# Kernel tuning notes

Measured on AMD Instinct MI355X. Metric: run time of the kernel, lower is better.

## Reference

```python
import jax, jax.numpy as jnp
import numpy as np

NEG_SLOPE = 0.2  # PyG GATConv default negative_slope
NUM_GRAPHS = 64


def gat_conv(x, src, dst, W, a_src, a_dst, bias, concat):
    """PyG-style GATConv (eval mode, self-loops already appended to src/dst)."""
    N = x.shape[0]
    H, C = a_src.shape
    h = (x @ W).reshape(N, H, C)                      # [N,H,C]
    al_s = jnp.sum(h * a_src, axis=-1)                # [N,H]
    al_d = jnp.sum(h * a_dst, axis=-1)                # [N,H]
    e = jax.nn.leaky_relu(al_s[src] + al_d[dst], NEG_SLOPE)  # [E,H]
    # numerically-stable segment softmax over incoming edges of each dst node
    m = jax.ops.segment_max(e, dst, num_segments=N)   # [N,H]
    ex = jnp.exp(e - m[dst])
    denom = jax.ops.segment_sum(ex, dst, num_segments=N)
    alpha = ex / (denom[dst] + 1e-16)                 # [E,H]
    out = jax.ops.segment_sum(h[src] * alpha[:, :, None], dst, num_segments=N)  # [N,H,C]
    out = out.reshape(N, H * C) if concat else out.mean(axis=1)
    return out + bias


def setup_inputs() -> dict:
    key = jax.random.key(0)
    ks = jax.random.split(key, 32)
    N, E, F_in, H = 20000, 100000, 128, 8
    x = jax.random.normal(ks[0], (N, F_in), jnp.float32)
    edge_index = jax.random.randint(ks[1], (2, E), 0, N, dtype=jnp.int32)
    batch = jnp.sort(jax.random.randint(ks[2], (N,), 0, NUM_GRAPHS, dtype=jnp.int32))
    inp = {"x": x, "edge_index": edge_index, "batch": batch}
    # (fan_in, per-head channels) for conv1..conv_final
    dims = [(F_in, 64), (512, 256), (2048, 256), (2048, 256), (2048, 256)]
    ki = 3
    for i, (fi, c) in enumerate(dims, 1):
        concat = i < 5
        inp[f"W{i}"] = jax.random.normal(ks[ki], (fi, H * c), jnp.float32) * (1.0 / np.sqrt(fi)); ki += 1
        inp[f"a_src{i}"] = jax.random.normal(ks[ki], (H, c), jnp.float32) * 0.1; ki += 1
        inp[f"a_dst{i}"] = jax.random.normal(ks[ki], (H, c), jnp.float32) * 0.1; ki += 1
        inp[f"b{i}"] = jnp.zeros((H * c if concat else c,), jnp.float32)
    inp["W_lin"] = jax.random.normal(ks[ki], (256, 128), jnp.float32) * (1.0 / np.sqrt(256))
    inp["b_lin"] = jnp.zeros((128,), jnp.float32)
    return inp


def reference(x, edge_index, batch,
              W1, a_src1, a_dst1, b1,
              W2, a_src2, a_dst2, b2,
              W3, a_src3, a_dst3, b3,
              W4, a_src4, a_dst4, b4,
              W5, a_src5, a_dst5, b5,
              W_lin, b_lin):
    N = x.shape[0]
    loop = jnp.arange(N, dtype=edge_index.dtype)  # GATConv add_self_loops=True
    src = jnp.concatenate([edge_index[0], loop])
    dst = jnp.concatenate([edge_index[1], loop])
    h = jax.nn.elu(gat_conv(x, src, dst, W1, a_src1, a_dst1, b1, True))
    h = jax.nn.elu(gat_conv(h, src, dst, W2, a_src2, a_dst2, b2, True))
    h = jax.nn.elu(gat_conv(h, src, dst, W3, a_src3, a_dst3, b3, True))
    h = jax.nn.elu(gat_conv(h, src, dst, W4, a_src4, a_dst4, b4, True))
    h = jax.nn.elu(gat_conv(h, src, dst, W5, a_src5, a_dst5, b5, False))
    sums = jax.ops.segment_sum(h, batch, num_segments=NUM_GRAPHS)
    counts = jax.ops.segment_sum(jnp.ones((N, 1), h.dtype), batch, num_segments=NUM_GRAPHS)
    pooled = jax.nn.elu(sums / jnp.maximum(counts, 1.0))  # global_mean_pool + elu
    return pooled @ W_lin + b_lin
```

## Files before the change

### kernel.cpp

```cpp
#include <hip/hip_runtime.h>
#include <hip/hip_fp16.h>
#include <math.h>

#define NHEADS 8
#define NG 64

typedef _Float16 half8_t __attribute__((ext_vector_type(8)));
typedef _Float16 half4_t __attribute__((ext_vector_type(4)));
typedef float    float4_t __attribute__((ext_vector_type(4)));
typedef __attribute__((address_space(1))) const void g_void;
typedef __attribute__((address_space(3))) void l_void;

__device__ __forceinline__ float elu_f(float x)   { return x > 0.f ? x : expf(x) - 1.f; }
__device__ __forceinline__ float lrelu_f(float x) { return x >= 0.f ? x : 0.2f * x; }

__device__ __forceinline__ float4 ld4(const float* p) { return *(const float4*)p; }
__device__ __forceinline__ float4 ld4(const __half* p) {
    const __half2* q = (const __half2*)p;
    __half2 a = q[0], b = q[1];
    return make_float4(__half2float(a.x), __half2float(a.y),
                       __half2float(b.x), __half2float(b.y));
}
__device__ __forceinline__ void st4(float* p, float4 v) { *(float4*)p = v; }
__device__ __forceinline__ void st4(__half* p, float4 v) {
    __half2 a, b;
    a.x = __float2half(v.x); a.y = __float2half(v.y);
    b.x = __float2half(v.z); b.y = __float2half(v.w);
    __half2* q = (__half2*)p; q[0] = a; q[1] = b;
}
__device__ __forceinline__ float scl(float v)  { return v; }
__device__ __forceinline__ float scl(__half v) { return __half2float(v); }
__device__ __forceinline__ void sst(float* p, float v)  { *p = v; }
__device__ __forceinline__ void sst(__half* p, float v) { *p = __float2half(v); }

__global__ void hist_kernel(const int* __restrict__ ei, int E, int Etot, int* __restrict__ counts) {
    int e = blockIdx.x * blockDim.x + threadIdx.x;
    if (e >= Etot) return;
    int dst = (e < E) ? ei[E + e] : (e - E);
    atomicAdd(&counts[dst], 1);
}

__global__ void scan_kernel(const int* __restrict__ counts, int* __restrict__ offsets,
                            int* __restrict__ cursor, int N) {
    __shared__ int sdata[256];
    __shared__ int carry_s;
    if (threadIdx.x == 0) carry_s = 0;
    __syncthreads();
    for (int base = 0; base < N; base += 256) {
        int i = base + (int)threadIdx.x;
        int v = (i < N) ? counts[i] : 0;
        sdata[threadIdx.x] = v;
        __syncthreads();
        for (int off = 1; off < 256; off <<= 1) {
            int t = (threadIdx.x >= (unsigned)off) ? sdata[threadIdx.x - off] : 0;
            __syncthreads();
            sdata[threadIdx.x] += t;
            __syncthreads();
        }
        int excl = sdata[threadIdx.x] - v + carry_s;
        if (i < N) { offsets[i] = excl; cursor[i] = excl; }
        __syncthreads();
        if (threadIdx.x == 255) carry_s += sdata[255];
        __syncthreads();
    }
    if (threadIdx.x == 0) offsets[N] = carry_s;
}

__global__ void scatter_kernel(const int* __restrict__ ei, int E, int Etot,
                               int* __restrict__ cursor, int* __restrict__ perm_src) {
    int e = blockIdx.x * blockDim.x + threadIdx.x;
    if (e >= Etot) return;
    int src, dst;
    if (e < E) { src = ei[e]; dst = ei[E + e]; }
    else       { src = e - E; dst = e - E; }
    int pos = atomicAdd(&cursor[dst], 1);
    perm_src[pos] = src;
}

__global__ __launch_bounds__(256) void transpose_conv_kernel(const float* __restrict__ W,
                                                             __half* __restrict__ Wt,
                                                             int K, int N) {
    __shared__ float t[32][33];
    int nb = blockIdx.x * 32, kb = blockIdx.y * 32;
    int tx = threadIdx.x & 31, ty = threadIdx.x >> 5;
#pragma unroll
    for (int r = 0; r < 32; r += 8)
        t[ty + r][tx] = W[(size_t)(kb + ty + r) * N + nb + tx];
    __syncthreads();
#pragma unroll
    for (int r = 0; r < 32; r += 8)
        Wt[(size_t)(nb + ty + r) * K + kb + tx] = __float2half(t[tx][ty + r]);
}

struct h4s { __half a, b, c, d; };
__global__ void f32_to_f16_kernel(const float* __restrict__ in, __half* __restrict__ out, long n4) {
    long i = (long)blockIdx.x * blockDim.x + threadIdx.x;
    if (i >= n4) return;
    float4 v = ((const float4*)in)[i];
    h4s o; o.a = __float2half(v.x); o.b = __float2half(v.y);
    o.c = __float2half(v.z); o.d = __float2half(v.w);
    ((h4s*)out)[i] = o;
}

__global__ __launch_bounds__(256) void gemm_mfma_kernel(const __half* __restrict__ A,
                                                        const __half* __restrict__ Bt,
                                                        __half* __restrict__ C,
                                                        int M, int N, int K) {
    __shared__ __align__(16) __half Asm[128 * 64];
    __shared__ __align__(16) __half Bsm[128 * 64];
    const int tid  = threadIdx.x;
    const int lane = tid & 63;
    const int wave = tid >> 6;

    const int nwg = (int)(gridDim.x * gridDim.y);
    const int lin = (int)(blockIdx.y * gridDim.x + blockIdx.x);
    const int q = nwg >> 3, r = nwg & 7;
    const int xcd = lin & 7, idx = lin >> 3;
    const int nid = (xcd < r ? xcd * (q + 1) : r * (q + 1) + (xcd - r) * q) + idx;
    const int bx = nid % (int)gridDim.x;
    const int by = nid / (int)gridDim.x;
    const int row0 = by * 128;
    const int col0 = bx * 128;

    const int l15 = lane & 15;
    const int l4  = lane >> 4;
    const int wm  = (wave >> 1) * 64;
    const int wn  = (wave & 1) * 64;

    const int sl_row = lane >> 3;
    const int sl_kch = (lane & 7) ^ sl_row;

    float4_t acc[4][4];
#pragma unroll
    for (int i = 0; i < 4; ++i)
#pragma unroll
        for (int j = 0; j < 4; ++j)
            acc[i][j] = (float4_t){0.f, 0.f, 0.f, 0.f};

    for (int k0 = 0; k0 < K; k0 += 64) {
#pragma unroll
        for (int i = 0; i < 4; ++i) {
            int rr = (i * 4 + wave) * 8 + sl_row;
            int ar = row0 + rr; if (ar >= M) ar = M - 1;
            const __half* ga = A + (size_t)ar * K + k0 + sl_kch * 8;
            char* la = (char*)Asm + ((i * 4 + wave) * 1024 + lane * 16);
            __builtin_amdgcn_global_load_lds((g_void*)ga, (l_void*)la, 16, 0, 0);
            const __half* gb = Bt + (size_t)(col0 + rr) * K + k0 + sl_kch * 8;
            char* lb = (char*)Bsm + ((i * 4 + wave) * 1024 + lane * 16);
            __builtin_amdgcn_global_load_lds((g_void*)gb, (l_void*)lb, 16, 0, 0);
        }
        __syncthreads();
#pragma unroll
        for (int kh = 0; kh < 2; ++kh) {
            half8_t af[4], bf[4];
#pragma unroll
            for (int f = 0; f < 4; ++f) {
                int rowa = wm + f * 16 + l15;
                int ca = (kh * 4 + l4) ^ (rowa & 7);
                af[f] = *(const half8_t*)((const char*)Asm + rowa * 128 + ca * 16);
                int rowb = wn + f * 16 + l15;
                int cb = (kh * 4 + l4) ^ (rowb & 7);
                bf[f] = *(const half8_t*)((const char*)Bsm + rowb * 128 + cb * 16);
            }
#pragma unroll
            for (int fm = 0; fm < 4; ++fm)
#pragma unroll
                for (int fn = 0; fn < 4; ++fn)
                    acc[fm][fn] = __builtin_amdgcn_mfma_f32_16x16x32_f16(af[fm], bf[fn], acc[fm][fn], 0, 0, 0);
        }
        __syncthreads();
    }

#pragma unroll
    for (int fm = 0; fm < 4; ++fm) {
#pragma unroll
        for (int r2 = 0; r2 < 4; ++r2) {
            int row = row0 + wm + fm * 16 + l4 * 4 + r2;
            if (row < M) {
#pragma unroll
                for (int fn = 0; fn < 4; ++fn) {
                    int col = col0 + wn + fn * 16 + l15;
                    C[(size_t)row * N + col] = __float2half(acc[fm][fn][r2]);
                }
            }
        }
    }
}

template <typename TA, typename TC>
__global__ __launch_bounds__(256) void gemm_kernel(const TA* __restrict__ A,
                                                   const float* __restrict__ B,
                                                   TC* __restrict__ C,
                                                   int M, int N, int K) {
    __shared__ float As[16][64];
    __shared__ float Bs[16][64];
    const int tid  = threadIdx.x;
    const int row0 = blockIdx.y * 64, col0 = blockIdx.x * 64;
    const int am = tid >> 2, ak = (tid & 3) << 2;
    const int bk = tid >> 4, bn = (tid & 15) << 2;
    const int ty = (tid >> 4) << 2, tx = (tid & 15) << 2;
    float acc[4][4] = {};
    const int arow = row0 + am;
    for (int k0 = 0; k0 < K; k0 += 16) {
        float4 a4 = make_float4(0.f, 0.f, 0.f, 0.f);
        if (arow < M) a4 = ld4(A + (size_t)arow * K + k0 + ak);
        As[ak + 0][am] = a4.x; As[ak + 1][am] = a4.y;
        As[ak + 2][am] = a4.z; As[ak + 3][am] = a4.w;
        *(float4*)&Bs[bk][bn] = *(const float4*)(B + (size_t)(k0 + bk) * N + col0 + bn);
        __syncthreads();
#pragma unroll
        for (int k = 0; k < 16; ++k) {
            float4 ar = *(const float4*)&As[k][ty];
            float4 br = *(const float4*)&Bs[k][tx];
            acc[0][0] += ar.x * br.x; acc[0][1] += ar.x * br.y; acc[0][2] += ar.x * br.z; acc[0][3] += ar.x * br.w;
            acc[1][0] += ar.y * br.x; acc[1][1] += ar.y * br.y; acc[1][2] += ar.y * br.z; acc[1][3] += ar.y * br.w;
            acc[2][0] += ar.z * br.x; acc[2][1] += ar.z * br.y; acc[2][2] += ar.z * br.z; acc[2][3] += ar.z * br.w;
            acc[3][0] += ar.w * br.x; acc[3][1] += ar.w * br.y; acc[3][2] += ar.w * br.z; acc[3][3] += ar.w * br.w;
        }
        __syncthreads();
    }
#pragma unroll
    for (int i = 0; i < 4; ++i) {
        int r = row0 + ty + i;
        if (r < M) {
            float4 o = make_float4(acc[i][0], acc[i][1], acc[i][2], acc[i][3]);
            st4(C + (size_t)r * N + col0 + tx, o);
        }
    }
}

template <int C>
__global__ void al_vec_kernel(const __half* __restrict__ ht, const float* __restrict__ a_src,
                              const float* __restrict__ a_dst, float* __restrict__ al_s,
                              float* __restrict__ al_d, int N) {
    int wid  = (int)((blockIdx.x * blockDim.x + threadIdx.x) >> 6);
    int lane = threadIdx.x & 63;
    if (wid >= N * NHEADS) return;
    int n = wid / NHEADS, h = wid % NHEADS;
    float ss = 0.f, sd = 0.f;
    int c0 = lane * 4;
    if (c0 < C) {
        const __half* hp = ht + (size_t)n * (NHEADS * C) + h * C + c0;
        half4_t v = *(const half4_t*)hp;
        float4 as4 = *(const float4*)(a_src + h * C + c0);
        float4 ad4 = *(const float4*)(a_dst + h * C + c0);
        float v0 = (float)v[0], v1 = (float)v[1], v2 = (float)v[2], v3 = (float)v[3];
        ss = v0 * as4.x + v1 * as4.y + v2 * as4.z + v3 * as4.w;
        sd = v0 * ad4.x + v1 * ad4.y + v2 * ad4.z + v3 * ad4.w;
    }
#pragma unroll
    for (int off = 32; off > 0; off >>= 1) {
        ss += __shfl_down(ss, off);
        sd += __shfl_down(sd, off);
    }
    if (lane == 0) { al_s[wid] = ss; al_d[wid] = sd; }
}

__global__ void alpha_node_kernel(const int* __restrict__ offsets, const int* __restrict__ perm_src,
                                  const float* __restrict__ al_s, const float* __restrict__ al_d,
                                  float* __restrict__ alpha, float* __restrict__ inv_d, int N) {
    int n = blockIdx.x * blockDim.x + threadIdx.x;
    if (n >= N) return;
    int s = offsets[n], e = offsets[n + 1];
    float ad[8], m[8], den[8];
    {
        float4 d0 = *(const float4*)(al_d + (size_t)n * 8);
        float4 d1 = *(const float4*)(al_d + (size_t)n * 8 + 4);
        ad[0] = d0.x; ad[1] = d0.y; ad[2] = d0.z; ad[3] = d0.w;
        ad[4] = d1.x; ad[5] = d1.y; ad[6] = d1.z; ad[7] = d1.w;
    }
#pragma unroll
    for (int h = 0; h < 8; ++h) { m[h] = -1e30f; den[h] = 0.f; }
    for (int p = s; p < e; ++p) {
        int src = perm_src[p];
        float4 s0 = *(const float4*)(al_s + (size_t)src * 8);
        float4 s1 = *(const float4*)(al_s + (size_t)src * 8 + 4);
        float as8[8] = {s0.x, s0.y, s0.z, s0.w, s1.x, s1.y, s1.z, s1.w};
#pragma unroll
        for (int h = 0; h < 8; ++h) m[h] = fmaxf(m[h], lrelu_f(as8[h] + ad[h]));
    }
    for (int p = s; p < e; ++p) {
        int src = perm_src[p];
        float4 s0 = *(const float4*)(al_s + (size_t)src * 8);
        float4 s1 = *(const float4*)(al_s + (size_t)src * 8 + 4);
        float as8[8] = {s0.x, s0.y, s0.z, s0.w, s1.x, s1.y, s1.z, s1.w};
        float ex8[8];
#pragma unroll
        for (int h = 0; h < 8; ++h) {
            float ex = expf(lrelu_f(as8[h] + ad[h]) - m[h]);
            ex8[h] = ex; den[h] += ex;
        }
        float4* ap = (float4*)(alpha + (size_t)p * 8);
        ap[0] = make_float4(ex8[0], ex8[1], ex8[2], ex8[3]);
        ap[1] = make_float4(ex8[4], ex8[5], ex8[6], ex8[7]);
    }
    float4* ip = (float4*)(inv_d + (size_t)n * 8);
    ip[0] = make_float4(1.f / (den[0] + 1e-16f), 1.f / (den[1] + 1e-16f),
                        1.f / (den[2] + 1e-16f), 1.f / (den[3] + 1e-16f));
    ip[1] = make_float4(1.f / (den[4] + 1e-16f), 1.f / (den[5] + 1e-16f),
                        1.f / (den[6] + 1e-16f), 1.f / (den[7] + 1e-16f));
}

template <int HC, int C, int MODE>
__global__ __launch_bounds__(256) void agg_vec_kernel(const __half* __restrict__ ht,
                                                      const float* __restrict__ alpha,
                                                      const float* __restrict__ inv_d,
                                                      const int* __restrict__ offsets,
                                                      const int* __restrict__ perm_src,
                                                      const float* __restrict__ bias,
                                                      void* __restrict__ outv, int N) {
    constexpr int V = HC / 256;
    int n = blockIdx.x;
    int tid = threadIdx.x;
    const int head = (tid * V) / C;
    float acc[V];
#pragma unroll
    for (int i = 0; i < V; ++i) acc[i] = 0.f;
    int s = offsets[n], e = offsets[n + 1];
    const __half* base = ht + (size_t)tid * V;
    for (int p = s; p < e; ++p) {
        int src = perm_src[p];
        float a = alpha[(size_t)p * NHEADS + head];
        const __half* hp = base + (size_t)src * HC;
        if (V == 8) {
            half8_t v = *(const half8_t*)hp;
#pragma unroll
            for (int i = 0; i < 8; ++i) acc[i] += a * (float)v[i];
        } else {
            __half2 v2 = *(const __half2*)hp;
            acc[0] += a * __half2float(v2.x);
            acc[1] += a * __half2float(v2.y);
        }
    }
    float inv = inv_d[(size_t)n * NHEADS + head];
    if (MODE == 0) {
        __half* out = (__half*)outv;
        if (V == 8) {
            half8_t o;
#pragma unroll
            for (int i = 0; i < 8; ++i)
                o[i] = (_Float16)elu_f(acc[i] * inv + bias[tid * 8 + i]);
            *(half8_t*)(out + (size_t)n * HC + tid * 8) = o;
        } else {
            __half2 o;
            o.x = __float2half(elu_f(acc[0] * inv + bias[tid * 2 + 0]));
            o.y = __float2half(elu_f(acc[1] * inv + bias[tid * 2 + 1]));
            *(__half2*)(out + (size_t)n * HC + tid * 2) = o;
        }
    } else {
        __shared__ float sm[256][8];
#pragma unroll
        for (int i = 0; i < 8; ++i) sm[tid][i] = acc[i] * inv;
        __syncthreads();
        float ssum = 0.f;
#pragma unroll
        for (int h = 0; h < 8; ++h) ssum += sm[h * 32 + (tid >> 3)][tid & 7];
        float* out = (float*)outv;
        out[(size_t)n * C + tid] = elu_f(ssum * (1.f / NHEADS) + bias[tid]);
    }
}

template <typename TH>
__global__ void al_kernel(const TH* __restrict__ ht, const float* __restrict__ a_src,
                          const float* __restrict__ a_dst, float* __restrict__ al_s,
                          float* __restrict__ al_d, int N, int C) {
    int wid  = (int)((blockIdx.x * blockDim.x + threadIdx.x) >> 6);
    int lane = threadIdx.x & 63;
    if (wid >= N * NHEADS) return;
    int n = wid / NHEADS, h = wid % NHEADS;
    const TH* hp = ht + (size_t)n * (NHEADS * C) + h * C;
    float ss = 0.f, sd = 0.f;
    for (int c = lane; c < C; c += 64) {
        float v = scl(hp[c]);
        ss += v * a_src[h * C + c];
        sd += v * a_dst[h * C + c];
    }
#pragma unroll
    for (int off = 32; off > 0; off >>= 1) {
        ss += __shfl_down(ss, off);
        sd += __shfl_down(sd, off);
    }
    if (lane == 0) { al_s[wid] = ss; al_d[wid] = sd; }
}

__global__ void alpha_kernel(const int* __restrict__ offsets, const int* __restrict__ perm_src,
                             const float* __restrict__ al_s, const float* __restrict__ al_d,
                             float* __restrict__ alpha, int N) {
    int idx = blockIdx.x * blockDim.x + threadIdx.x;
    if (idx >= N * NHEADS) return;
    int n = idx / NHEADS, h = idx % NHEADS;
    int s = offsets[n], e = offsets[n + 1];
    float ad = al_d[idx];
    float m = -1e30f;
    for (int p = s; p < e; ++p) {
        float v = lrelu_f(al_s[perm_src[p] * NHEADS + h] + ad);
        m = fmaxf(m, v);
    }
    float denom = 0.f;
    for (int p = s; p < e; ++p) {
        float v  = lrelu_f(al_s[perm_src[p] * NHEADS + h] + ad);
        float ex = expf(v - m);
        alpha[(size_t)p * NHEADS + h] = ex;
        denom += ex;
    }
    float inv = 1.f / (denom + 1e-16f);
    for (int p = s; p < e; ++p) alpha[(size_t)p * NHEADS + h] *= inv;
}

template <int HC, int C, int MODE, typename TH, typename TO>
__global__ __launch_bounds__(256) void agg_kernel(const TH* __restrict__ ht,
                                                  const float* __restrict__ alpha,
                                                  const int* __restrict__ offsets,
                                                  const int* __restrict__ perm_src,
                                                  const float* __restrict__ bias,
                                                  TO* __restrict__ out, int N) {
    constexpr int PER = HC / 256;
    int n = blockIdx.x;
    int tid = threadIdx.x;
    float acc[PER];
#pragma unroll
    for (int i = 0; i < PER; ++i) acc[i] = 0.f;
    int s = offsets[n], e = offsets[n + 1];
    for (int p = s; p < e; ++p) {
        int src = perm_src[p];
        const TH* hp = ht + (size_t)src * HC;
#pragma unroll
        for (int i = 0; i < PER; ++i) {
            int j = tid + i * 256;
            float a = alpha[(size_t)p * NHEADS + (j / C)];
            acc[i] += a * scl(hp[j]);
        }
    }
    if (MODE == 0) {
#pragma unroll
        for (int i = 0; i < PER; ++i) {
            int j = tid + i * 256;
            sst(&out[(size_t)n * HC + j], elu_f(acc[i] + bias[j]));
        }
    } else {
        float srow = 0.f;
#pragma unroll
        for (int i = 0; i < PER; ++i) srow += acc[i];
        sst(&out[(size_t)n * C + tid], elu_f(srow * (1.f / NHEADS) + bias[tid]));
    }
}

__global__ void gstart_kernel(const int* __restrict__ batch, int* __restrict__ gstart, int N) {
    int n = blockIdx.x * blockDim.x + threadIdx.x;
    if (n > N) return;
    if (n == 0) {
        int b0 = batch[0];
        for (int g = 0; g <= b0; ++g) gstart[g] = 0;
    } else if (n == N) {
        int bl = batch[N - 1];
        for (int g = bl + 1; g <= NG; ++g) gstart[g] = N;
    } else {
        int bp = batch[n - 1], bc = batch[n];
        for (int g = bp + 1; g <= bc; ++g) gstart[g] = n;
    }
}

__global__ void pool_kernel(const float* __restrict__ h5, const int* __restrict__ gstart,
                            float* __restrict__ pooled) {
    int g = blockIdx.x, c = threadIdx.x;
    int s = gstart[g], e = gstart[g + 1];
    float sum = 0.f;
    for (int n = s; n < e; ++n) sum += h5[(size_t)n * 256 + c];
    float cnt = fmaxf((float)(e - s), 1.f);
    pooled[g * 256 + c] = elu_f(sum / cnt);
}

__global__ void linear_kernel(const float* __restrict__ pooled, const float* __restrict__ W,
                              const float* __restrict__ b, float* __restrict__ out) {
    int g = blockIdx.x, c = threadIdx.x;
    float s = b[c];
    for (int k = 0; k < 256; ++k) s += pooled[g * 256 + k] * W[k * 128 + c];
    out[g * 128 + c] = s;
}

template <typename TIO, typename TH>
static void run_pipeline(const float* x, const float* const* W, const float* const* asrc,
                         const float* const* adst, const float* const* bias,
                         char* rawIO, char* rawHT,
                         float* al_s, float* al_d, float* alpha_buf,
                         const int* offsets, const int* perm_src,
                         int N, hipStream_t stream) {
    TIO* bufIO = (TIO*)rawIO;
    TH*  bufHT = (TH*)rawHT;
    {
        dim3 g(512 / 64, (N + 63) / 64);
        gemm_kernel<float, TH><<<g, 256, 0, stream>>>(x, W[0], bufHT, N, 512, 128);
        al_kernel<TH><<<(N * NHEADS * 64 + 255) / 256, 256, 0, stream>>>(bufHT, asrc[0], adst[0], al_s, al_d, N, 64);
        alpha_kernel<<<(N * NHEADS + 255) / 256, 256, 0, stream>>>(offsets, perm_src, al_s, al_d, alpha_buf, N);
        agg_kernel<512, 64, 0, TH, TIO><<<N, 256, 0, stream>>>(bufHT, alpha_buf, offsets, perm_src, bias[0], bufIO, N);
    }
    int Kdim = 512;
    for (int l = 1; l < 5; ++l) {
        dim3 g(2048 / 64, (N + 63) / 64);
        gemm_kernel<TIO, TH><<<g, 256, 0, stream>>>(bufIO, W[l], bufHT, N, 2048, Kdim);
        al_kernel<TH><<<(N * NHEADS * 64 + 255) / 256, 256, 0, stream>>>(bufHT, asrc[l], adst[l], al_s, al_d, N, 256);
        alpha_kernel<<<(N * NHEADS + 255) / 256, 256, 0, stream>>>(offsets, perm_src, al_s, al_d, alpha_buf, N);
        if (l < 4)
            agg_kernel<2048, 256, 0, TH, TIO><<<N, 256, 0, stream>>>(bufHT, alpha_buf, offsets, perm_src, bias[l], bufIO, N);
        else
            agg_kernel<2048, 256, 1, TH, float><<<N, 256, 0, stream>>>(bufHT, alpha_buf, offsets, perm_src, bias[l], (float*)rawIO, N);
        Kdim = 2048;
    }
}

extern "C" void kernel_launch(void* const* d_in, const int* in_sizes, int n_in,
                              void* d_out, int out_size, void* d_ws, size_t ws_size,
                              hipStream_t stream) {
    const float* x     = (const float*)d_in[0];
    const int*   ei    = (const int*)d_in[1];
    const int*   batch = (const int*)d_in[2];
    const float* W[5]    = {(const float*)d_in[3],  (const float*)d_in[7],  (const float*)d_in[11],
                            (const float*)d_in[15], (const float*)d_in[19]};
    const float* asrc[5] = {(const float*)d_in[4],  (const float*)d_in[8],  (const float*)d_in[12],
                            (const float*)d_in[16], (const float*)d_in[20]};
    const float* adst[5] = {(const float*)d_in[5],  (const float*)d_in[9],  (const float*)d_in[13],
                            (const float*)d_in[17], (const float*)d_in[21]};
    const float* bias[5] = {(const float*)d_in[6],  (const float*)d_in[10], (const float*)d_in[14],
                            (const float*)d_in[18], (const float*)d_in[22]};
    const float* Wlin = (const float*)d_in[23];
    const float* blin = (const float*)d_in[24];

    const int N    = in_sizes[0] / 128;
    const int E    = in_sizes[1] / 2;
    const int Etot = E + N;

    auto align256 = [](size_t b) { return (b + 255) & ~(size_t)255; };

    size_t sz_counts = align256((size_t)N * 4);
    size_t sz_off    = align256((size_t)(N + 1) * 4);
    size_t sz_cur    = align256((size_t)N * 4);
    size_t sz_perm   = align256((size_t)Etot * 4);
    size_t sz_al     = align256((size_t)N * NHEADS * 4);
    size_t sz_alpha  = align256((size_t)Etot * NHEADS * 4);
    size_t sz_inv    = align256((size_t)N * NHEADS * 4);
    size_t sz_gst    = align256((size_t)(NG + 1) * 4);
    size_t sz_pool   = align256((size_t)NG * 256 * 4);
    size_t misc = sz_counts + sz_off + sz_cur + sz_perm + 2 * sz_al + sz_alpha + sz_inv + sz_gst + sz_pool;

    size_t bigf  = align256((size_t)N * 2048 * sizeof(float));
    size_t bigh  = align256((size_t)N * 2048 * sizeof(__half));
    size_t sz_wt  = align256((size_t)2048 * 2048 * sizeof(__half));
    size_t sz_x16 = align256((size_t)N * 128 * sizeof(__half));

    int path;
    if      (ws_size >= misc + 2 * bigh + sz_wt + sz_x16) path = 3;
    else if (ws_size >= misc + 2 * bigf)                  path = 0;
    else if (ws_size >= misc + bigf + bigh)               path = 1;
    else if (ws_size >= misc + 2 * bigh)                  path = 2;
    else {
        hipMemsetAsync(d_out, 0, (size_t)out_size * sizeof(float), stream);
        return;
    }

    char* ws = (char*)d_ws;
    size_t off = 0;
    auto carve = [&](size_t bytes) { void* p = ws + off; off += bytes; return p; };
    int*   counts   = (int*)carve(sz_counts);
    int*   offsets  = (int*)carve(sz_off);
    int*   cursor   = (int*)carve(sz_cur);
    int*   perm_src = (int*)carve(sz_perm);
    float* al_s     = (float*)carve(sz_al);
    float* al_d     = (float*)carve(sz_al);
    float* alpha    = (float*)carve(sz_alpha);
    float* inv_d    = (float*)carve(sz_inv);
    int*   gstart   = (int*)carve(sz_gst);
    float* pooled   = (float*)carve(sz_pool);

    hipMemsetAsync(counts, 0, (size_t)N * 4, stream);
    hist_kernel<<<(Etot + 255) / 256, 256, 0, stream>>>(ei, E, Etot, counts);
    scan_kernel<<<1, 256, 0, stream>>>(counts, offsets, cursor, N);
    scatter_kernel<<<(Etot + 255) / 256, 256, 0, stream>>>(ei, E, Etot, cursor, perm_src);

    if (path == 3) {
        char*   rawIO = (char*)carve(bigh);
        char*   rawHT = (char*)carve(bigh);
        __half* Wt    = (__half*)carve(sz_wt);
        __half* x16   = (__half*)carve(sz_x16);
        __half* bufIO = (__half*)rawIO;
        __half* bufHT = (__half*)rawHT;

        long n4 = (long)N * 128 / 4;
        f32_to_f16_kernel<<<(int)((n4 + 255) / 256), 256, 0, stream>>>(x, x16, n4);

        const __half* curA = x16;
        int Kdim = 128;
        for (int l = 0; l < 5; ++l) {
            const int C  = (l == 0) ? 64 : 256;
            const int HC = NHEADS * C;
            {
                dim3 tg(HC / 32, Kdim / 32);
                transpose_conv_kernel<<<tg, 256, 0, stream>>>(W[l], Wt, Kdim, HC);
            }
            {
                dim3 gg(HC / 128, (N + 127) / 128);
                gemm_mfma_kernel<<<gg, 256, 0, stream>>>(curA, Wt, bufHT, N, HC, Kdim);
            }
            if (l == 0)
                al_vec_kernel<64><<<(N * NHEADS * 64 + 255) / 256, 256, 0, stream>>>(bufHT, asrc[l], adst[l], al_s, al_d, N);
            else
                al_vec_kernel<256><<<(N * NHEADS * 64 + 255) / 256, 256, 0, stream>>>(bufHT, asrc[l], adst[l], al_s, al_d, N);
            alpha_node_kernel<<<(N + 255) / 256, 256, 0, stream>>>(offsets, perm_src, al_s, al_d, alpha, inv_d, N);
            if (l == 0)
                agg_vec_kernel<512, 64, 0><<<N, 256, 0, stream>>>(bufHT, alpha, inv_d, offsets, perm_src, bias[l], bufIO, N);
            else if (l < 4)
                agg_vec_kernel<2048, 256, 0><<<N, 256, 0, stream>>>(bufHT, alpha, inv_d, offsets, perm_src, bias[l], bufIO, N);
            else
                agg_vec_kernel<2048, 256, 1><<<N, 256, 0, stream>>>(bufHT, alpha, inv_d, offsets, perm_src, bias[l], (float*)rawIO, N);
            curA = bufIO;
            Kdim = (l == 0) ? 512 : 2048;
        }
        gstart_kernel<<<(N + 1 + 255) / 256, 256, 0, stream>>>(batch, gstart, N);
        pool_kernel<<<NG, 256, 0, stream>>>((const float*)rawIO, gstart, pooled);
        linear_kernel<<<NG, 128, 0, stream>>>(pooled, Wlin, blin, (float*)d_out);
        return;
    }

    char* rawIO = (char*)carve(path == 2 ? bigh : bigf);
    char* rawHT = (char*)carve(path == 0 ? bigf : bigh);

    if (path == 0)
        run_pipeline<float, float>(x, W, asrc, adst, bias, rawIO, rawHT, al_s, al_d, alpha, offsets, perm_src, N, stream);
    else if (path == 1)
        run_pipeline<float, __half>(x, W, asrc, adst, bias, rawIO, rawHT, al_s, al_d, alpha, offsets, perm_src, N, stream);
    else
        run_pipeline<__half, __half>(x, W, asrc, adst, bias, rawIO, rawHT, al_s, al_d, alpha, offsets, perm_src, N, stream);

    gstart_kernel<<<(N + 1 + 255) / 256, 256, 0, stream>>>(batch, gstart, N);
    pool_kernel<<<NG, 256, 0, stream>>>((const float*)rawIO, gstart, pooled);
    linear_kernel<<<NG, 128, 0, stream>>>(pooled, Wlin, blin, (float*)d_out);
}
```

Baseline: 1.425 ms.

## Batch weight prep, wave-parallel softmax, faster scan, unrolled aggregation, fused pool+linear

Several changes at once. The x conversion and all five weight transposes now run in a single prep launch, with one buffer per layer. The single-block scan uses wave shuffles with four elements per thread. The per-node softmax kernel is replaced by one wave per node that splits edges and heads across lanes. The aggregation loop is unrolled by four so gathers overlap, and pooling and the final linear layer are fused into one kernel that finds graph bounds by binary search. Together these cut launch count and serial latency, at the cost of more workspace for the per-layer weight buffers.

```diff
diff --git a/kernel.cpp b/kernel.cpp
--- a/kernel.cpp
+++ b/kernel.cpp
@@ -33,6 +33,8 @@
 __device__ __forceinline__ void sst(float* p, float v)  { *p = v; }
 __device__ __forceinline__ void sst(__half* p, float v) { *p = __float2half(v); }
 
+struct h4s { __half a, b, c, d; };
+
 __global__ void hist_kernel(const int* __restrict__ ei, int E, int Etot, int* __restrict__ counts) {
     int e = blockIdx.x * blockDim.x + threadIdx.x;
     if (e >= Etot) return;
@@ -40,30 +42,46 @@
     atomicAdd(&counts[dst], 1);
 }
 
-__global__ void scan_kernel(const int* __restrict__ counts, int* __restrict__ offsets,
-                            int* __restrict__ cursor, int N) {
-    __shared__ int sdata[256];
-    __shared__ int carry_s;
-    if (threadIdx.x == 0) carry_s = 0;
-    __syncthreads();
-    for (int base = 0; base < N; base += 256) {
-        int i = base + (int)threadIdx.x;
-        int v = (i < N) ? counts[i] : 0;
-        sdata[threadIdx.x] = v;
+__global__ __launch_bounds__(256) void scan_kernel(const int* __restrict__ counts,
+                                                   int* __restrict__ offsets,
+                                                   int* __restrict__ cursor, int N) {
+    __shared__ int wsum[4];
+    const int tid = threadIdx.x;
+    const int lane = tid & 63, wid = tid >> 6;
+    int carry = 0;
+    for (int base = 0; base < N; base += 1024) {
+        int i0 = base + tid * 4;
+        int v0 = 0, v1 = 0, v2 = 0, v3 = 0;
+        if (i0 + 3 < N) {
+            int4 q = *(const int4*)(counts + i0);
+            v0 = q.x; v1 = q.y; v2 = q.z; v3 = q.w;
+        } else {
+            if (i0     < N) v0 = counts[i0];
+            if (i0 + 1 < N) v1 = counts[i0 + 1];
+            if (i0 + 2 < N) v2 = counts[i0 + 2];
+            if (i0 + 3 < N) v3 = counts[i0 + 3];
+        }
+        int tsum = v0 + v1 + v2 + v3;
+        int incl = tsum;
+#pragma unroll
+        for (int off = 1; off < 64; off <<= 1) {
+            int t = __shfl_up(incl, off);
+            if (lane >= off) incl += t;
+        }
+        if (lane == 63) wsum[wid] = incl;
         __syncthreads();
-        for (int off = 1; off < 256; off <<= 1) {
-            int t = (threadIdx.x >= (unsigned)off) ? sdata[threadIdx.x - off] : 0;
-            __syncthreads();
-            sdata[threadIdx.x] += t;
-            __syncthreads();
-        }
-        int excl = sdata[threadIdx.x] - v + carry_s;
-        if (i < N) { offsets[i] = excl; cursor[i] = excl; }
+        int woff = carry;
+        for (int w = 0; w < wid; ++w) woff += wsum[w];
+        int o0 = woff + incl - tsum;
+        int o1 = o0 + v0, o2 = o1 + v1, o3 = o2 + v2;
+        if (i0     < N) { offsets[i0]     = o0; cursor[i0]     = o0; }
+        if (i0 + 1 < N) { offsets[i0 + 1] = o1; cursor[i0 + 1] = o1; }
+        if (i0 + 2 < N) { offsets[i0 + 2] = o2; cursor[i0 + 2] = o2; }
+        if (i0 + 3 < N) { offsets[i0 + 3] = o3; cursor[i0 + 3] = o3; }
         __syncthreads();
-        if (threadIdx.x == 255) carry_s += sdata[255];
-        __syncthreads();
-    }
-    if (threadIdx.x == 0) offsets[N] = carry_s;
+        carry += wsum[0] + wsum[1] + wsum[2] + wsum[3];
+    }
+    if (tid == 0) offsets[N] = carry;
 }
 
 __global__ void scatter_kernel(const int* __restrict__ ei, int E, int Etot,
@@ -77,29 +95,44 @@
     perm_src[pos] = src;
 }
 
-__global__ __launch_bounds__(256) void transpose_conv_kernel(const float* __restrict__ W,
-                                                             __half* __restrict__ Wt,
-                                                             int K, int N) {
-    __shared__ float t[32][33];
-    int nb = blockIdx.x * 32, kb = blockIdx.y * 32;
+struct PrepArgs {
+    const float* x; __half* x16; long n4;
+    const float* W0; const float* W1; const float* W2; const float* W3; const float* W4;
+    __half* T0; __half* T1; __half* T2; __half* T3; __half* T4;
+    int K0, K1, K2, K3, K4;
+    int N0, N1, N2, N3, N4;
+    int b0, b1, b2, b3, b4, b5;
+};
+
+__global__ __launch_bounds__(256) void prep_kernel(PrepArgs a) {
+    int bid = blockIdx.x;
+    if (bid < a.b0) {
+        long i = (long)bid * 256 + threadIdx.x;
+        if (i < a.n4) {
+            float4 v = ((const float4*)a.x)[i];
+            h4s o; o.a = __float2half(v.x); o.b = __float2half(v.y);
+            o.c = __float2half(v.z); o.d = __float2half(v.w);
+            ((h4s*)a.x16)[i] = o;
+        }
+        return;
+    }
+    const float* W; __half* T; int K, Nn, t;
+    if      (bid < a.b1) { W = a.W0; T = a.T0; K = a.K0; Nn = a.N0; t = bid - a.b0; }
+    else if (bid < a.b2) { W = a.W1; T = a.T1; K = a.K1; Nn = a.N1; t = bid - a.b1; }
+    else if (bid < a.b3) { W = a.W2; T = a.T2; K = a.K2; Nn = a.N2; t = bid - a.b2; }
+    else if (bid < a.b4) { W = a.W3; T = a.T3; K = a.K3; Nn = a.N3; t = bid - a.b3; }
+    else                 { W = a.W4; T = a.T4; K = a.K4; Nn = a.N4; t = bid - a.b4; }
+    int tilesx = Nn >> 5;
+    int nb = (t % tilesx) * 32, kb = (t / tilesx) * 32;
+    __shared__ float tt[32][33];
     int tx = threadIdx.x & 31, ty = threadIdx.x >> 5;
 #pragma unroll
     for (int r = 0; r < 32; r += 8)
-        t[ty + r][tx] = W[(size_t)(kb + ty + r) * N + nb + tx];
+        tt[ty + r][tx] = W[(size_t)(kb + ty + r) * Nn + nb + tx];
     __syncthreads();
 #pragma unroll
     for (int r = 0; r < 32; r += 8)
-        Wt[(size_t)(nb + ty + r) * K + kb + tx] = __float2half(t[tx][ty + r]);
-}
-
-struct h4s { __half a, b, c, d; };
-__global__ void f32_to_f16_kernel(const float* __restrict__ in, __half* __restrict__ out, long n4) {
-    long i = (long)blockIdx.x * blockDim.x + threadIdx.x;
-    if (i >= n4) return;
-    float4 v = ((const float4*)in)[i];
-    h4s o; o.a = __float2half(v.x); o.b = __float2half(v.y);
-    o.c = __float2half(v.z); o.d = __float2half(v.w);
-    ((h4s*)out)[i] = o;
+        T[(size_t)(nb + ty + r) * K + kb + tx] = __float2half(tt[tx][ty + r]);
 }
 
 __global__ __launch_bounds__(256) void gemm_mfma_kernel(const __half* __restrict__ A,
@@ -256,49 +289,42 @@
     if (lane == 0) { al_s[wid] = ss; al_d[wid] = sd; }
 }
 
-__global__ void alpha_node_kernel(const int* __restrict__ offsets, const int* __restrict__ perm_src,
-                                  const float* __restrict__ al_s, const float* __restrict__ al_d,
-                                  float* __restrict__ alpha, float* __restrict__ inv_d, int N) {
-    int n = blockIdx.x * blockDim.x + threadIdx.x;
-    if (n >= N) return;
+__global__ __launch_bounds__(256) void alpha_wave_kernel(const int* __restrict__ offsets,
+                                                         const int* __restrict__ perm_src,
+                                                         const float* __restrict__ al_s,
+                                                         const float* __restrict__ al_d,
+                                                         float* __restrict__ alpha,
+                                                         float* __restrict__ inv_d, int N) {
+    int wid  = (int)((blockIdx.x * blockDim.x + threadIdx.x) >> 6);
+    int lane = threadIdx.x & 63;
+    if (wid >= N) return;
+    int n = wid;
+    int h = lane & 7, es = lane >> 3;
     int s = offsets[n], e = offsets[n + 1];
-    float ad[8], m[8], den[8];
-    {
-        float4 d0 = *(const float4*)(al_d + (size_t)n * 8);
-        float4 d1 = *(const float4*)(al_d + (size_t)n * 8 + 4);
-        ad[0] = d0.x; ad[1] = d0.y; ad[2] = d0.z; ad[3] = d0.w;
-        ad[4] = d1.x; ad[5] = d1.y; ad[6] = d1.z; ad[7] = d1.w;
-    }
-#pragma unroll
-    for (int h = 0; h < 8; ++h) { m[h] = -1e30f; den[h] = 0.f; }
-    for (int p = s; p < e; ++p) {
-        int src = perm_src[p];
-        float4 s0 = *(const float4*)(al_s + (size_t)src * 8);
-        float4 s1 = *(const float4*)(al_s + (size_t)src * 8 + 4);
-        float as8[8] = {s0.x, s0.y, s0.z, s0.w, s1.x, s1.y, s1.z, s1.w};
-#pragma unroll
-        for (int h = 0; h < 8; ++h) m[h] = fmaxf(m[h], lrelu_f(as8[h] + ad[h]));
-    }
-    for (int p = s; p < e; ++p) {
-        int src = perm_src[p];
-        float4 s0 = *(const float4*)(al_s + (size_t)src * 8);
-        float4 s1 = *(const float4*)(al_s + (size_t)src * 8 + 4);
-        float as8[8] = {s0.x, s0.y, s0.z, s0.w, s1.x, s1.y, s1.z, s1.w};
-        float ex8[8];
-#pragma unroll
-        for (int h = 0; h < 8; ++h) {
-            float ex = expf(lrelu_f(as8[h] + ad[h]) - m[h]);
-            ex8[h] = ex; den[h] += ex;
-        }
-        float4* ap = (float4*)(alpha + (size_t)p * 8);
-        ap[0] = make_float4(ex8[0], ex8[1], ex8[2], ex8[3]);
-        ap[1] = make_float4(ex8[4], ex8[5], ex8[6], ex8[7]);
-    }
-    float4* ip = (float4*)(inv_d + (size_t)n * 8);
-    ip[0] = make_float4(1.f / (den[0] + 1e-16f), 1.f / (den[1] + 1e-16f),
-                        1.f / (den[2] + 1e-16f), 1.f / (den[3] + 1e-16f));
-    ip[1] = make_float4(1.f / (den[4] + 1e-16f), 1.f / (den[5] + 1e-16f),
-                        1.f / (den[6] + 1e-16f), 1.f / (den[7] + 1e-16f));
+    float ad = al_d[(size_t)n * 8 + h];
+    float m = -1e30f;
+    for (int p0 = s; p0 < e; p0 += 8) {
+        int p = p0 + es;
+        if (p < e) {
+            int src = perm_src[p];
+            m = fmaxf(m, lrelu_f(al_s[(size_t)src * 8 + h] + ad));
+        }
+    }
+#pragma unroll
+    for (int off = 8; off < 64; off <<= 1) m = fmaxf(m, __shfl_xor(m, off));
+    float den = 0.f;
+    for (int p0 = s; p0 < e; p0 += 8) {
+        int p = p0 + es;
+        if (p < e) {
+            int src = perm_src[p];
+            float ex = expf(lrelu_f(al_s[(size_t)src * 8 + h] + ad) - m);
+            alpha[(size_t)p * 8 + h] = ex;
+            den += ex;
+        }
+    }
+#pragma unroll
+    for (int off = 8; off < 64; off <<= 1) den += __shfl_xor(den, off);
+    if (es == 0) inv_d[(size_t)n * 8 + h] = 1.f / (den + 1e-16f);
 }
 
 template <int HC, int C, int MODE>
@@ -318,9 +344,39 @@
     for (int i = 0; i < V; ++i) acc[i] = 0.f;
     int s = offsets[n], e = offsets[n + 1];
     const __half* base = ht + (size_t)tid * V;
-    for (int p = s; p < e; ++p) {
+    const float* ap = alpha + head;
+    int p = s;
+    for (; p + 4 <= e; p += 4) {
+        int s0 = perm_src[p], s1 = perm_src[p + 1], s2 = perm_src[p + 2], s3 = perm_src[p + 3];
+        float a0 = ap[(size_t)p * 8],       a1 = ap[(size_t)(p + 1) * 8];
+        float a2 = ap[(size_t)(p + 2) * 8], a3 = ap[(size_t)(p + 3) * 8];
+        if (V == 8) {
+            half8_t v0 = *(const half8_t*)(base + (size_t)s0 * HC);
+            half8_t v1 = *(const half8_t*)(base + (size_t)s1 * HC);
+            half8_t v2 = *(const half8_t*)(base + (size_t)s2 * HC);
+            half8_t v3 = *(const half8_t*)(base + (size_t)s3 * HC);
+#pragma unroll
+            for (int i = 0; i < 8; ++i) acc[i] += a0 * (float)v0[i];
+#pragma unroll
+            for (int i = 0; i < 8; ++i) acc[i] += a1 * (float)v1[i];
+#pragma unroll
+            for (int i = 0; i < 8; ++i) acc[i] += a2 * (float)v2[i];
+#pragma unroll
+            for (int i = 0; i < 8; ++i) acc[i] += a3 * (float)v3[i];
+        } else {
+            __half2 w0 = *(const __half2*)(base + (size_t)s0 * HC);
+            __half2 w1 = *(const __half2*)(base + (size_t)s1 * HC);
+            __half2 w2 = *(const __half2*)(base + (size_t)s2 * HC);
+            __half2 w3 = *(const __half2*)(base + (size_t)s3 * HC);
+            acc[0] += a0 * __half2float(w0.x); acc[1] += a0 * __half2float(w0.y);
+            acc[0] += a1 * __half2float(w1.x); acc[1] += a1 * __half2float(w1.y);
+            acc[0] += a2 * __half2float(w2.x); acc[1] += a2 * __half2float(w2.y);
+            acc[0] += a3 * __half2float(w3.x); acc[1] += a3 * __half2float(w3.y);
+        }
+    }
+    for (; p < e; ++p) {
         int src = perm_src[p];
-        float a = alpha[(size_t)p * NHEADS + head];
+        float a = ap[(size_t)p * 8];
         const __half* hp = base + (size_t)src * HC;
         if (V == 8) {
             half8_t v = *(const half8_t*)hp;
@@ -476,6 +532,33 @@
     float s = b[c];
     for (int k = 0; k < 256; ++k) s += pooled[g * 256 + k] * W[k * 128 + c];
     out[g * 128 + c] = s;
+}
+
+__device__ __forceinline__ int lb_dev(const int* a, int n, int key) {
+    int lo = 0, hi = n;
+    while (lo < hi) { int mid = (lo + hi) >> 1; if (a[mid] < key) lo = mid + 1; else hi = mid; }
+    return lo;
+}
+
+__global__ __launch_bounds__(256) void pool_linear_kernel(const float* __restrict__ h5,
+                                                          const int* __restrict__ batch, int N,
+                                                          const float* __restrict__ Wlin,
+                                                          const float* __restrict__ blin,
+                                                          float* __restrict__ out) {
+    int g = blockIdx.x, c = threadIdx.x;
+    int s = lb_dev(batch, N, g);
+    int e = lb_dev(batch, N, g + 1);
+    __shared__ float pooled_s[256];
+    float sum = 0.f;
+    for (int n = s; n < e; ++n) sum += h5[(size_t)n * 256 + c];
+    float cnt = fmaxf((float)(e - s), 1.f);
+    pooled_s[c] = elu_f(sum / cnt);
+    __syncthreads();
+    if (c < 128) {
+        float acc = blin[c];
+        for (int k = 0; k < 256; ++k) acc += pooled_s[k] * Wlin[k * 128 + c];
+        out[g * 128 + c] = acc;
+    }
 }
 
 template <typename TIO, typename TH>
@@ -544,14 +627,17 @@
 
     size_t bigf  = align256((size_t)N * 2048 * sizeof(float));
     size_t bigh  = align256((size_t)N * 2048 * sizeof(__half));
-    size_t sz_wt  = align256((size_t)2048 * 2048 * sizeof(__half));
+    const int Kd[5] = {128, 512, 2048, 2048, 2048};
+    const int Nd[5] = {512, 2048, 2048, 2048, 2048};
+    size_t sz_wt_each[5], sz_wt_all = 0;
+    for (int l = 0; l < 5; ++l) { sz_wt_each[l] = align256((size_t)Kd[l] * Nd[l] * sizeof(__half)); sz_wt_all += sz_wt_each[l]; }
     size_t sz_x16 = align256((size_t)N * 128 * sizeof(__half));
 
     int path;
-    if      (ws_size >= misc + 2 * bigh + sz_wt + sz_x16) path = 3;
-    else if (ws_size >= misc + 2 * bigf)                  path = 0;
-    else if (ws_size >= misc + bigf + bigh)               path = 1;
-    else if (ws_size >= misc + 2 * bigh)                  path = 2;
+    if      (ws_size >= misc + 2 * bigh + sz_wt_all + sz_x16) path = 3;
+    else if (ws_size >= misc + 2 * bigf)                      path = 0;
+    else if (ws_size >= misc + bigf + bigh)                   path = 1;
+    else if (ws_size >= misc + 2 * bigh)                      path = 2;
     else {
         hipMemsetAsync(d_out, 0, (size_t)out_size * sizeof(float), stream);
         return;
@@ -579,13 +665,24 @@
     if (path == 3) {
         char*   rawIO = (char*)carve(bigh);
         char*   rawHT = (char*)carve(bigh);
-        __half* Wt    = (__half*)carve(sz_wt);
+        __half* Wt[5];
+        for (int l = 0; l < 5; ++l) Wt[l] = (__half*)carve(sz_wt_each[l]);
         __half* x16   = (__half*)carve(sz_x16);
         __half* bufIO = (__half*)rawIO;
         __half* bufHT = (__half*)rawHT;
 
-        long n4 = (long)N * 128 / 4;
-        f32_to_f16_kernel<<<(int)((n4 + 255) / 256), 256, 0, stream>>>(x, x16, n4);
+        PrepArgs pa;
+        pa.x = x; pa.x16 = x16; pa.n4 = (long)N * 128 / 4;
+        pa.W0 = W[0]; pa.W1 = W[1]; pa.W2 = W[2]; pa.W3 = W[3]; pa.W4 = W[4];
+        pa.T0 = Wt[0]; pa.T1 = Wt[1]; pa.T2 = Wt[2]; pa.T3 = Wt[3]; pa.T4 = Wt[4];
+        pa.K0 = Kd[0]; pa.K1 = Kd[1]; pa.K2 = Kd[2]; pa.K3 = Kd[3]; pa.K4 = Kd[4];
+        pa.N0 = Nd[0]; pa.N1 = Nd[1]; pa.N2 = Nd[2]; pa.N3 = Nd[3]; pa.N4 = Nd[4];
+        int bacc = (int)((pa.n4 + 255) / 256);
+        pa.b0 = bacc;
+        int bends[5];
+        for (int l = 0; l < 5; ++l) { bacc += (Nd[l] / 32) * (Kd[l] / 32); bends[l] = bacc; }
+        pa.b1 = bends[0]; pa.b2 = bends[1]; pa.b3 = bends[2]; pa.b4 = bends[3]; pa.b5 = bends[4];
+        prep_kernel<<<pa.b5, 256, 0, stream>>>(pa);
 
         const __half* curA = x16;
         int Kdim = 128;
@@ -593,18 +690,14 @@
             const int C  = (l == 0) ? 64 : 256;
             const int HC = NHEADS * C;
             {
-                dim3 tg(HC / 32, Kdim / 32);
-                transpose_conv_kernel<<<tg, 256, 0, stream>>>(W[l], Wt, Kdim, HC);
-            }
-            {
                 dim3 gg(HC / 128, (N + 127) / 128);
-                gemm_mfma_kernel<<<gg, 256, 0, stream>>>(curA, Wt, bufHT, N, HC, Kdim);
+                gemm_mfma_kernel<<<gg, 256, 0, stream>>>(curA, Wt[l], bufHT, N, HC, Kdim);
             }
             if (l == 0)
                 al_vec_kernel<64><<<(N * NHEADS * 64 + 255) / 256, 256, 0, stream>>>(bufHT, asrc[l], adst[l], al_s, al_d, N);
             else
                 al_vec_kernel<256><<<(N * NHEADS * 64 + 255) / 256, 256, 0, stream>>>(bufHT, asrc[l], adst[l], al_s, al_d, N);
-            alpha_node_kernel<<<(N + 255) / 256, 256, 0, stream>>>(offsets, perm_src, al_s, al_d, alpha, inv_d, N);
+            alpha_wave_kernel<<<(N * 64 + 255) / 256, 256, 0, stream>>>(offsets, perm_src, al_s, al_d, alpha, inv_d, N);
             if (l == 0)
                 agg_vec_kernel<512, 64, 0><<<N, 256, 0, stream>>>(bufHT, alpha, inv_d, offsets, perm_src, bias[l], bufIO, N);
             else if (l < 4)
@@ -614,9 +707,7 @@
             curA = bufIO;
             Kdim = (l == 0) ? 512 : 2048;
         }
-        gstart_kernel<<<(N + 1 + 255) / 256, 256, 0, stream>>>(batch, gstart, N);
-        pool_kernel<<<NG, 256, 0, stream>>>((const float*)rawIO, gstart, pooled);
-        linear_kernel<<<NG, 128, 0, stream>>>(pooled, Wlin, blin, (float*)d_out);
+        pool_linear_kernel<<<NG, 256, 0, stream>>>((const float*)rawIO, batch, N, Wlin, blin, (float*)d_out);
         return;
     }
 
```

Measured after the change: 1.284 ms. 9.9% less time.
